# Performance work log

Measured on AMD Instinct MI355X. Metric: run time of the kernel, lower is better.

## Reference

```python
import jax, jax.numpy as jnp
import numpy as np

B, L, ENC_DIM, DEC_DIM, ATTN_DIM = 64, 2048, 1024, 1024, 512


def setup_inputs() -> dict:
    key = jax.random.key(0)
    ks = jax.random.split(key, 8)
    s_enc = 1.0 / np.sqrt(ENC_DIM)
    s_dec = 1.0 / np.sqrt(DEC_DIM)
    s_full = 1.0 / np.sqrt(ATTN_DIM)
    return {
        "encoder_out": jax.random.normal(ks[0], (B, L, ENC_DIM), jnp.float32),
        "decoder_hidden": jax.random.normal(ks[1], (B, DEC_DIM), jnp.float32),
        "We_w": jax.random.uniform(ks[2], (ENC_DIM, ATTN_DIM), jnp.float32, -s_enc, s_enc),
        "We_b": jax.random.uniform(ks[3], (ATTN_DIM,), jnp.float32, -s_enc, s_enc),
        "Wd_w": jax.random.uniform(ks[4], (DEC_DIM, ATTN_DIM), jnp.float32, -s_dec, s_dec),
        "Wd_b": jax.random.uniform(ks[5], (ATTN_DIM,), jnp.float32, -s_dec, s_dec),
        "Wf_w": jax.random.uniform(ks[6], (ATTN_DIM,), jnp.float32, -s_full, s_full),
        "Wf_b": jax.random.uniform(ks[7], (), jnp.float32, -s_full, s_full),
    }


def reference(encoder_out, decoder_hidden, We_w, We_b, Wd_w, Wd_b, Wf_w, Wf_b):
    # enc_attn: [B, L, A]; dec_attn: [B, A]
    enc_attn = jnp.einsum("ble,ea->bla", encoder_out, We_w) + We_b
    dec_attn = decoder_hidden @ Wd_w + Wd_b
    # additive score -> scalar per (B, L)
    hidden = jax.nn.relu(enc_attn + dec_attn[:, None, :])
    attn = jnp.einsum("bla,a->bl", hidden, Wf_w) + Wf_b
    alpha = jax.nn.softmax(attn, axis=1)  # over sequence dim
    weighted = jnp.einsum("ble,bl->be", encoder_out, alpha)
    return (weighted, alpha)
```

## Files before the change

### kernel.cpp

```cpp
#include <hip/hip_runtime.h>
#include <stdint.h>

#define B_BATCH 64
#define L_SEQ 2048
#define E_DIM 1024
#define A_DIM 512

typedef __attribute__((ext_vector_type(4))) float f32x4;
typedef __attribute__((ext_vector_type(8))) short bf16x8;
typedef __attribute__((ext_vector_type(2))) unsigned int u32x2;
typedef __attribute__((ext_vector_type(4))) unsigned int u32x4;

__device__ __forceinline__ unsigned short f2bf(float f) {
  unsigned u = __float_as_uint(f);
  u = (u + 0x7fffu + ((u >> 16) & 1u)) >> 16;
  return (unsigned short)u;
}

__device__ __forceinline__ u32x2 packbf(f32x4 v) {
  u32x2 r;
  r.x = (unsigned)f2bf(v.x) | ((unsigned)f2bf(v.y) << 16);
  r.y = (unsigned)f2bf(v.z) | ((unsigned)f2bf(v.w) << 16);
  return r;
}

#define BUFB 8192
#define BCHUNK 32768

__global__ void prep_we_kernel(const float* __restrict__ We, char* __restrict__ wsB) {
  int t = blockIdx.x * 256 + threadIdx.x;
  int lane = t & 63;
  int colblk = (t >> 6) & 31;
  int step = t >> 11;
  int nl = lane & 15, g = lane >> 4;
  int col = colblk * 16 + nl;
  int k0 = step * 32 + 4 * g;
  unsigned q0 = (unsigned)f2bf(We[(size_t)(k0 + 0) * A_DIM + col]) |
                ((unsigned)f2bf(We[(size_t)(k0 + 1) * A_DIM + col]) << 16);
  unsigned q1 = (unsigned)f2bf(We[(size_t)(k0 + 2) * A_DIM + col]) |
                ((unsigned)f2bf(We[(size_t)(k0 + 3) * A_DIM + col]) << 16);
  unsigned q2 = (unsigned)f2bf(We[(size_t)(k0 + 16) * A_DIM + col]) |
                ((unsigned)f2bf(We[(size_t)(k0 + 17) * A_DIM + col]) << 16);
  unsigned q3 = (unsigned)f2bf(We[(size_t)(k0 + 18) * A_DIM + col]) |
                ((unsigned)f2bf(We[(size_t)(k0 + 19) * A_DIM + col]) << 16);
  u32x4 v; v.x = q0; v.y = q1; v.z = q2; v.w = q3;
  *(u32x4*)(wsB + (size_t)t * 16) = v;
}

__global__ void dec_comb_kernel(const float* __restrict__ dh, const float* __restrict__ Wd,
                                const float* __restrict__ Wdb, const float* __restrict__ Web,
                                float* __restrict__ dcomb) {
  __shared__ float sh[1024];
  const int b = blockIdx.x, tid = threadIdx.x;
  for (int i = tid; i < 1024; i += 256) sh[i] = dh[b * 1024 + i];
  __syncthreads();
  const int a = blockIdx.y * 256 + tid;
  float acc = Wdb[a] + Web[a];
#pragma unroll 4
  for (int e = 0; e < 1024; ++e) acc += sh[e] * Wd[(size_t)e * A_DIM + a];
  dcomb[b * A_DIM + a] = acc;
}

__global__ __launch_bounds__(512, 2) void score_gemm_kernel(
    const float* __restrict__ enc, const char* __restrict__ wsB,
    const float* __restrict__ dcomb, const float* __restrict__ wf,
    float* __restrict__ scoreOut) {
  __shared__ __align__(16) char smem[3 * BUFB];
  __shared__ float s_score[128];

  const int tid = threadIdx.x;
  const int lane = tid & 63;
  const int w = tid >> 6;
  const int g = lane >> 4;
  const int nl = lane & 15;
  const int gs = g ^ ((nl >> 1) & 3);

  const int row0 = (int)blockIdx.x * 128;
  const int bb = row0 >> 11;

  if (tid < 128) s_score[tid] = 0.0f;

  const float* encA = enc + (size_t)row0 * E_DIM;

  int aoff[8];
#pragma unroll
  for (int rt = 0; rt < 8; ++rt) aoff[rt] = (rt * 16 + nl) * 64 + gs * 16;

  const int ar = tid >> 2, ag = tid & 3;
  const int aw = ar * 64 + ((ag ^ ((ar >> 1) & 3)) * 16);
  const float* asrc = encA + (size_t)ar * E_DIM + ag * 4;

  const char* bsrc = wsB + (w * 4) * 1024 + lane * 16;

  f32x4 acc[8][4];
#pragma unroll
  for (int rt = 0; rt < 8; ++rt)
#pragma unroll
    for (int ct = 0; ct < 4; ++ct) {
      f32x4 z = {0.f, 0.f, 0.f, 0.f};
      acc[rt][ct] = z;
    }
  f32x4 ra[2][2];
  bf16x8 bfr[2][4];

#define LOAD_A(kb_, s_)                                  \
  do {                                                   \
    ra[s_][0] = *(const f32x4*)(asrc + (kb_) * 32);      \
    ra[s_][1] = *(const f32x4*)(asrc + (kb_) * 32 + 16); \
  } while (0)

#define LOAD_B(kb_, s_)                                                     \
  do {                                                                      \
    _Pragma("unroll") for (int ct = 0; ct < 4; ++ct) bfr[s_][ct] =          \
        *(const bf16x8*)(bsrc + (size_t)(kb_)*BCHUNK + ct * 1024);          \
  } while (0)

#define WRITE_A(s_, dst_)                                          \
  do {                                                             \
    u32x2 l0 = packbf(ra[s_][0]);                                  \
    u32x2 h0 = packbf(ra[s_][1]);                                  \
    u32x4 w0; w0.x = l0.x; w0.y = l0.y; w0.z = h0.x; w0.w = h0.y;  \
    *(u32x4*)(smem + (dst_) + aw) = w0;                            \
  } while (0)

#define COMPUTE(cur_, s_)                                                    \
  do {                                                                       \
    bf16x8 afr[8];                                                           \
    _Pragma("unroll") for (int rt = 0; rt < 8; ++rt) afr[rt] =               \
        *(const bf16x8*)(smem + (cur_) + aoff[rt]);                          \
    __builtin_amdgcn_s_setprio(1);                                           \
    _Pragma("unroll") for (int rt = 0; rt < 8; ++rt)                         \
        _Pragma("unroll") for (int ct = 0; ct < 4; ++ct) acc[rt][ct] =       \
            __builtin_amdgcn_mfma_f32_16x16x32_bf16(afr[rt], bfr[s_][ct],    \
                                                    acc[rt][ct], 0, 0, 0);   \
    __builtin_amdgcn_s_setprio(0);                                           \
  } while (0)

  LOAD_A(0, 0);
  LOAD_A(1, 1);
  LOAD_B(0, 0);
  asm volatile("s_waitcnt vmcnt(6)" ::: "memory");
  WRITE_A(0, 0);

  int b0 = 0, b1 = BUFB, b2 = 2 * BUFB;
#pragma unroll 6
  for (int t = 0; t < 30; ++t) {
    LOAD_A(t + 2, t & 1);
    LOAD_B(t + 1, (t + 1) & 1);
    asm volatile("s_waitcnt vmcnt(6)" ::: "memory");
    WRITE_A((t + 1) & 1, b1);
    asm volatile("s_waitcnt lgkmcnt(0)" ::: "memory");
    asm volatile("s_barrier" ::: "memory");
    COMPUTE(b0, t & 1);
    int tmp = b0; b0 = b1; b1 = b2; b2 = tmp;
  }
  LOAD_B(31, 1);
  asm volatile("s_waitcnt vmcnt(4)" ::: "memory");
  WRITE_A(1, b1);
  asm volatile("s_waitcnt lgkmcnt(0)" ::: "memory");
  asm volatile("s_barrier" ::: "memory");
  COMPUTE(b0, 0);
  { int tmp = b0; b0 = b1; b1 = b2; b2 = tmp; }
  asm volatile("s_waitcnt vmcnt(0) lgkmcnt(0)" ::: "memory");
  asm volatile("s_barrier" ::: "memory");
  COMPUTE(b0, 1);

#undef LOAD_A
#undef LOAD_B
#undef WRITE_A
#undef COMPUTE

  float db[4], wv[4];
#pragma unroll
  for (int ct = 0; ct < 4; ++ct) {
    int a = w * 64 + ct * 16 + nl;
    db[ct] = dcomb[bb * A_DIM + a];
    wv[ct] = wf[a];
  }
#pragma unroll
  for (int rt = 0; rt < 8; ++rt) {
#pragma unroll
    for (int r = 0; r < 4; ++r) {
      float p = 0.f;
#pragma unroll
      for (int ct = 0; ct < 4; ++ct) {
        float h = acc[rt][ct][r] + db[ct];
        h = h > 0.f ? h : 0.f;
        p += h * wv[ct];
      }
      p += __shfl_xor(p, 1);
      p += __shfl_xor(p, 2);
      p += __shfl_xor(p, 4);
      p += __shfl_xor(p, 8);
      if (nl == 0) atomicAdd(&s_score[rt * 16 + g * 4 + r], p);
    }
  }
  __syncthreads();
  if (tid < 128) scoreOut[row0 + tid] = s_score[tid];
}

__global__ void softmax_kernel(float* __restrict__ attn) {
  __shared__ float red[8];
  const int b = blockIdx.x, tid = threadIdx.x;
  float* p = attn + b * L_SEQ;
  float v[8];
  float m = -1e30f;
#pragma unroll
  for (int i = 0; i < 8; ++i) {
    v[i] = p[tid + i * 256];
    m = fmaxf(m, v[i]);
  }
#pragma unroll
  for (int off = 1; off < 64; off <<= 1) m = fmaxf(m, __shfl_xor(m, off));
  const int wid = tid >> 6;
  if ((tid & 63) == 0) red[wid] = m;
  __syncthreads();
  m = fmaxf(fmaxf(red[0], red[1]), fmaxf(red[2], red[3]));
  float s = 0.f;
#pragma unroll
  for (int i = 0; i < 8; ++i) {
    v[i] = __expf(v[i] - m);
    s += v[i];
  }
#pragma unroll
  for (int off = 1; off < 64; off <<= 1) s += __shfl_xor(s, off);
  __syncthreads();
  if ((tid & 63) == 0) red[4 + wid] = s;
  __syncthreads();
  const float inv = 1.0f / (red[4] + red[5] + red[6] + red[7]);
#pragma unroll
  for (int i = 0; i < 8; ++i) p[tid + i * 256] = v[i] * inv;
}

__global__ void weighted_kernel(const float* __restrict__ enc, const float* __restrict__ alpha,
                                float* __restrict__ outW) {
  __shared__ float sa[64];
  const int bid = blockIdx.x;
  const int b = bid >> 5, ls = bid & 31;
  const int tid = threadIdx.x;
  if (tid < 64) sa[tid] = alpha[b * L_SEQ + ls * 64 + tid];
  __syncthreads();
  const f32x4* ep = (const f32x4*)(enc + ((size_t)(b * L_SEQ + ls * 64)) * E_DIM) + tid;
  f32x4 acc = {0.f, 0.f, 0.f, 0.f};
#pragma unroll 8
  for (int il = 0; il < 64; ++il) {
    f32x4 v = ep[(size_t)il * 256];
    float al = sa[il];
    acc.x += al * v.x;
    acc.y += al * v.y;
    acc.z += al * v.z;
    acc.w += al * v.w;
  }
  float* o = outW + b * E_DIM + tid * 4;
  atomicAdd(o + 0, acc.x);
  atomicAdd(o + 1, acc.y);
  atomicAdd(o + 2, acc.z);
  atomicAdd(o + 3, acc.w);
}

extern "C" void kernel_launch(void* const* d_in, const int* in_sizes, int n_in,
                              void* d_out, int out_size, void* d_ws, size_t ws_size,
                              hipStream_t stream) {
  const float* enc = (const float*)d_in[0];
  const float* dh = (const float*)d_in[1];
  const float* WeW = (const float*)d_in[2];
  const float* WeB = (const float*)d_in[3];
  const float* WdW = (const float*)d_in[4];
  const float* WdB = (const float*)d_in[5];
  const float* WfW = (const float*)d_in[6];

  float* out = (float*)d_out;
  float* outW = out;
  float* attn = out + B_BATCH * E_DIM;

  char* wsB = (char*)d_ws;
  float* dcomb = (float*)((char*)d_ws + 32 * (size_t)BCHUNK);

  if (ws_size < 32 * (size_t)BCHUNK + (size_t)B_BATCH * A_DIM * sizeof(float)) return;

  hipMemsetAsync(outW, 0, (size_t)(B_BATCH * E_DIM) * sizeof(float), stream);
  prep_we_kernel<<<256, 256, 0, stream>>>(WeW, wsB);
  dec_comb_kernel<<<dim3(B_BATCH, 2), 256, 0, stream>>>(dh, WdW, WdB, WeB, dcomb);
  score_gemm_kernel<<<(B_BATCH * L_SEQ) / 128, 512, 0, stream>>>(enc, wsB, dcomb, WfW, attn);
  softmax_kernel<<<B_BATCH, 256, 0, stream>>>(attn);
  weighted_kernel<<<B_BATCH * 32, 256, 0, stream>>>(enc, attn, outW);
}
```

Baseline: 384.5 us.

## Deepen A-tile prefetch to four stages with narrower per-thread enc loads

The score GEMM pipeline moves from three LDS buffers with A prefetched two k-steps ahead to four LDS buffers with A prefetched four k-steps ahead. The per-thread enc load pattern also changes: each thread now loads two 16-byte chunks from rows 64 apart instead of two adjacent chunks, and writes two 8-byte bf16 packs. The aim is to hide more global-load latency on the fp32 encoder stream. In exchange it uses more LDS and registers (ra grows to 4x2 vectors), which could reduce occupancy under launch_bounds(512,2).

```diff
diff --git a/kernel.cpp b/kernel.cpp
--- a/kernel.cpp
+++ b/kernel.cpp
@@ -65,7 +65,7 @@
     const float* __restrict__ enc, const char* __restrict__ wsB,
     const float* __restrict__ dcomb, const float* __restrict__ wf,
     float* __restrict__ scoreOut) {
-  __shared__ __align__(16) char smem[3 * BUFB];
+  __shared__ __align__(16) char smem[4 * BUFB];
   __shared__ float s_score[128];
 
   const int tid = threadIdx.x;
@@ -86,9 +86,10 @@
 #pragma unroll
   for (int rt = 0; rt < 8; ++rt) aoff[rt] = (rt * 16 + nl) * 64 + gs * 16;
 
-  const int ar = tid >> 2, ag = tid & 3;
-  const int aw = ar * 64 + ((ag ^ ((ar >> 1) & 3)) * 16);
-  const float* asrc = encA + (size_t)ar * E_DIM + ag * 4;
+  const int ar = tid >> 3, c = tid & 7;
+  const int aw0 = ar * 64 + (((c & 3) ^ ((ar >> 1) & 3)) * 16) + (c >> 2) * 8;
+  const int aw1 = aw0 + 64 * 64;
+  const float* as0 = encA + (size_t)ar * E_DIM + c * 4;
 
   const char* bsrc = wsB + (w * 4) * 1024 + lane * 16;
 
@@ -100,30 +101,29 @@
       f32x4 z = {0.f, 0.f, 0.f, 0.f};
       acc[rt][ct] = z;
     }
-  f32x4 ra[2][2];
+  f32x4 ra[4][2];
   bf16x8 bfr[2][4];
 
-#define LOAD_A(kb_, s_)                                  \
-  do {                                                   \
-    ra[s_][0] = *(const f32x4*)(asrc + (kb_) * 32);      \
-    ra[s_][1] = *(const f32x4*)(asrc + (kb_) * 32 + 16); \
-  } while (0)
-
-#define LOAD_B(kb_, s_)                                                     \
-  do {                                                                      \
-    _Pragma("unroll") for (int ct = 0; ct < 4; ++ct) bfr[s_][ct] =          \
-        *(const bf16x8*)(bsrc + (size_t)(kb_)*BCHUNK + ct * 1024);          \
-  } while (0)
-
-#define WRITE_A(s_, dst_)                                          \
-  do {                                                             \
-    u32x2 l0 = packbf(ra[s_][0]);                                  \
-    u32x2 h0 = packbf(ra[s_][1]);                                  \
-    u32x4 w0; w0.x = l0.x; w0.y = l0.y; w0.z = h0.x; w0.w = h0.y;  \
-    *(u32x4*)(smem + (dst_) + aw) = w0;                            \
-  } while (0)
-
-#define COMPUTE(cur_, s_)                                                    \
+#define LOAD_A(kb_)                                                     \
+  do {                                                                  \
+    ra[(kb_) & 3][0] = *(const f32x4*)(as0 + (size_t)(kb_) * 32);       \
+    ra[(kb_) & 3][1] = *(const f32x4*)(as0 + (size_t)(kb_) * 32 +       \
+                                       (size_t)64 * E_DIM);             \
+  } while (0)
+
+#define LOAD_B(kb_)                                                     \
+  do {                                                                  \
+    _Pragma("unroll") for (int ct = 0; ct < 4; ++ct) bfr[(kb_) & 1][ct] = \
+        *(const bf16x8*)(bsrc + (size_t)(kb_)*BCHUNK + ct * 1024);      \
+  } while (0)
+
+#define WRITE_A(kb_, dst_)                                              \
+  do {                                                                  \
+    *(u32x2*)(smem + (dst_) + aw0) = packbf(ra[(kb_) & 3][0]);          \
+    *(u32x2*)(smem + (dst_) + aw1) = packbf(ra[(kb_) & 3][1]);          \
+  } while (0)
+
+#define COMPUTE(cur_, kb_)                                                   \
   do {                                                                       \
     bf16x8 afr[8];                                                           \
     _Pragma("unroll") for (int rt = 0; rt < 8; ++rt) afr[rt] =               \
@@ -131,39 +131,50 @@
     __builtin_amdgcn_s_setprio(1);                                           \
     _Pragma("unroll") for (int rt = 0; rt < 8; ++rt)                         \
         _Pragma("unroll") for (int ct = 0; ct < 4; ++ct) acc[rt][ct] =       \
-            __builtin_amdgcn_mfma_f32_16x16x32_bf16(afr[rt], bfr[s_][ct],    \
+            __builtin_amdgcn_mfma_f32_16x16x32_bf16(afr[rt], bfr[(kb_)&1][ct], \
                                                     acc[rt][ct], 0, 0, 0);   \
     __builtin_amdgcn_s_setprio(0);                                           \
   } while (0)
 
-  LOAD_A(0, 0);
-  LOAD_A(1, 1);
-  LOAD_B(0, 0);
-  asm volatile("s_waitcnt vmcnt(6)" ::: "memory");
+  LOAD_A(0);
+  LOAD_B(0);
+  LOAD_A(1);
+  LOAD_A(2);
+  LOAD_A(3);
+  asm volatile("s_waitcnt vmcnt(10)" ::: "memory");
   WRITE_A(0, 0);
 
-  int b0 = 0, b1 = BUFB, b2 = 2 * BUFB;
-#pragma unroll 6
-  for (int t = 0; t < 30; ++t) {
-    LOAD_A(t + 2, t & 1);
-    LOAD_B(t + 1, (t + 1) & 1);
-    asm volatile("s_waitcnt vmcnt(6)" ::: "memory");
-    WRITE_A((t + 1) & 1, b1);
+#pragma unroll 4
+  for (int t = 0; t < 28; ++t) {
+    LOAD_B(t + 1);
+    LOAD_A(t + 4);
+    asm volatile("s_waitcnt vmcnt(8)" ::: "memory");
+    WRITE_A(t + 1, ((t + 1) & 3) * BUFB);
     asm volatile("s_waitcnt lgkmcnt(0)" ::: "memory");
     asm volatile("s_barrier" ::: "memory");
-    COMPUTE(b0, t & 1);
-    int tmp = b0; b0 = b1; b1 = b2; b2 = tmp;
-  }
-  LOAD_B(31, 1);
+    COMPUTE((t & 3) * BUFB, t);
+  }
+  LOAD_B(29);
+  asm volatile("s_waitcnt vmcnt(6)" ::: "memory");
+  WRITE_A(29, 1 * BUFB);
+  asm volatile("s_waitcnt lgkmcnt(0)" ::: "memory");
+  asm volatile("s_barrier" ::: "memory");
+  COMPUTE(0 * BUFB, 28);
+  LOAD_B(30);
   asm volatile("s_waitcnt vmcnt(4)" ::: "memory");
-  WRITE_A(1, b1);
+  WRITE_A(30, 2 * BUFB);
   asm volatile("s_waitcnt lgkmcnt(0)" ::: "memory");
   asm volatile("s_barrier" ::: "memory");
-  COMPUTE(b0, 0);
-  { int tmp = b0; b0 = b1; b1 = b2; b2 = tmp; }
+  COMPUTE(1 * BUFB, 29);
+  LOAD_B(31);
+  asm volatile("s_waitcnt vmcnt(4)" ::: "memory");
+  WRITE_A(31, 3 * BUFB);
+  asm volatile("s_waitcnt lgkmcnt(0)" ::: "memory");
+  asm volatile("s_barrier" ::: "memory");
+  COMPUTE(2 * BUFB, 30);
   asm volatile("s_waitcnt vmcnt(0) lgkmcnt(0)" ::: "memory");
   asm volatile("s_barrier" ::: "memory");
-  COMPUTE(b0, 1);
+  COMPUTE(3 * BUFB, 31);
 
 #undef LOAD_A
 #undef LOAD_B
```

Result: no change. 386.3 us (+0.5%).

## Deepen score GEMM K-step to 64 with split B prefetch and replicated weight copies

Applied to the files above, without the earlier changes.

The score GEMM main loop now stages 64 K-elements of the encoder tile per barrier (two 32-wide chunks per LDS buffer) instead of 32. This halves the number of barriers and interleaves the B-fragment loads between the two MFMA chunks. The prepared bf16 weight buffer is also replicated 8 times in the workspace, and blocks pick a copy by blockIdx, to spread L2/channel contention on the shared weights. The cost is more workspace, a larger LDS footprint (48KB at 2 blocks/CU), and more registers for the A staging.

```diff
diff --git a/kernel.cpp b/kernel.cpp
--- a/kernel.cpp
+++ b/kernel.cpp
@@ -24,8 +24,10 @@
   return r;
 }
 
-#define BUFB 8192
+#define CHUNKB 8192
+#define BUFB 16384
 #define BCHUNK 32768
+#define BCOPY (32 * BCHUNK)
 
 __global__ void prep_we_kernel(const float* __restrict__ We, char* __restrict__ wsB) {
   int t = blockIdx.x * 256 + threadIdx.x;
@@ -44,7 +46,9 @@
   unsigned q3 = (unsigned)f2bf(We[(size_t)(k0 + 18) * A_DIM + col]) |
                 ((unsigned)f2bf(We[(size_t)(k0 + 19) * A_DIM + col]) << 16);
   u32x4 v; v.x = q0; v.y = q1; v.z = q2; v.w = q3;
-  *(u32x4*)(wsB + (size_t)t * 16) = v;
+#pragma unroll
+  for (int c = 0; c < 8; ++c)
+    *(u32x4*)(wsB + (size_t)c * BCOPY + (size_t)t * 16) = v;
 }
 
 __global__ void dec_comb_kernel(const float* __restrict__ dh, const float* __restrict__ Wd,
@@ -86,11 +90,11 @@
 #pragma unroll
   for (int rt = 0; rt < 8; ++rt) aoff[rt] = (rt * 16 + nl) * 64 + gs * 16;
 
-  const int ar = tid >> 2, ag = tid & 3;
-  const int aw = ar * 64 + ((ag ^ ((ar >> 1) & 3)) * 16);
-  const float* asrc = encA + (size_t)ar * E_DIM + ag * 4;
-
-  const char* bsrc = wsB + (w * 4) * 1024 + lane * 16;
+  const int ar = tid >> 2, ac = tid & 3;
+  const int aw = ar * 64 + ((ac ^ ((ar >> 1) & 3)) * 16);
+  const float* asrc = encA + (size_t)ar * E_DIM + ac * 4;
+
+  const char* bsrc = wsB + (size_t)(blockIdx.x & 7) * BCOPY + (w * 4) * 1024 + lane * 16;
 
   f32x4 acc[8][4];
 #pragma unroll
@@ -100,75 +104,87 @@
       f32x4 z = {0.f, 0.f, 0.f, 0.f};
       acc[rt][ct] = z;
     }
-  f32x4 ra[2][2];
-  bf16x8 bfr[2][4];
-
-#define LOAD_A(kb_, s_)                                  \
-  do {                                                   \
-    ra[s_][0] = *(const f32x4*)(asrc + (kb_) * 32);      \
-    ra[s_][1] = *(const f32x4*)(asrc + (kb_) * 32 + 16); \
+  f32x4 ra[4];
+  bf16x8 bfr0[4], bfr1[4];
+
+#define LOAD_A(t_)                                                       \
+  do {                                                                   \
+    _Pragma("unroll") for (int j = 0; j < 4; ++j)                        \
+        ra[j] = *(const f32x4*)(asrc + (size_t)(t_) * 64 + j * 16);      \
   } while (0)
 
-#define LOAD_B(kb_, s_)                                                     \
-  do {                                                                      \
-    _Pragma("unroll") for (int ct = 0; ct < 4; ++ct) bfr[s_][ct] =          \
-        *(const bf16x8*)(bsrc + (size_t)(kb_)*BCHUNK + ct * 1024);          \
+#define LOAD_B(kc_, dst_)                                                \
+  do {                                                                   \
+    _Pragma("unroll") for (int ct = 0; ct < 4; ++ct) dst_[ct] =          \
+        *(const bf16x8*)(bsrc + (size_t)(kc_)*BCHUNK + ct * 1024);       \
   } while (0)
 
-#define WRITE_A(s_, dst_)                                          \
-  do {                                                             \
-    u32x2 l0 = packbf(ra[s_][0]);                                  \
-    u32x2 h0 = packbf(ra[s_][1]);                                  \
-    u32x4 w0; w0.x = l0.x; w0.y = l0.y; w0.z = h0.x; w0.w = h0.y;  \
-    *(u32x4*)(smem + (dst_) + aw) = w0;                            \
+#define WRITE_A(dst_)                                                    \
+  do {                                                                   \
+    u32x2 l0 = packbf(ra[0]), h0 = packbf(ra[1]);                        \
+    u32x2 l1 = packbf(ra[2]), h1 = packbf(ra[3]);                        \
+    u32x4 w0; w0.x = l0.x; w0.y = l0.y; w0.z = h0.x; w0.w = h0.y;        \
+    u32x4 w1; w1.x = l1.x; w1.y = l1.y; w1.z = h1.x; w1.w = h1.y;        \
+    *(u32x4*)(smem + (dst_) + aw) = w0;                                  \
+    *(u32x4*)(smem + (dst_) + CHUNKB + aw) = w1;                         \
   } while (0)
 
-#define COMPUTE(cur_, s_)                                                    \
-  do {                                                                       \
-    bf16x8 afr[8];                                                           \
-    _Pragma("unroll") for (int rt = 0; rt < 8; ++rt) afr[rt] =               \
-        *(const bf16x8*)(smem + (cur_) + aoff[rt]);                          \
-    __builtin_amdgcn_s_setprio(1);                                           \
-    _Pragma("unroll") for (int rt = 0; rt < 8; ++rt)                         \
-        _Pragma("unroll") for (int ct = 0; ct < 4; ++ct) acc[rt][ct] =       \
-            __builtin_amdgcn_mfma_f32_16x16x32_bf16(afr[rt], bfr[s_][ct],    \
-                                                    acc[rt][ct], 0, 0, 0);   \
-    __builtin_amdgcn_s_setprio(0);                                           \
+#define MFMA_CHUNK(cur_, bfr_)                                           \
+  do {                                                                   \
+    bf16x8 afr[8];                                                       \
+    _Pragma("unroll") for (int rt = 0; rt < 8; ++rt) afr[rt] =           \
+        *(const bf16x8*)(smem + (cur_) + aoff[rt]);                      \
+    __builtin_amdgcn_s_setprio(1);                                       \
+    _Pragma("unroll") for (int rt = 0; rt < 8; ++rt)                     \
+        _Pragma("unroll") for (int ct = 0; ct < 4; ++ct) acc[rt][ct] =   \
+            __builtin_amdgcn_mfma_f32_16x16x32_bf16(afr[rt], bfr_[ct],   \
+                                                    acc[rt][ct], 0, 0, 0); \
+    __builtin_amdgcn_s_setprio(0);                                       \
   } while (0)
 
-  LOAD_A(0, 0);
-  LOAD_A(1, 1);
-  LOAD_B(0, 0);
-  asm volatile("s_waitcnt vmcnt(6)" ::: "memory");
-  WRITE_A(0, 0);
+  LOAD_A(0);
+  LOAD_B(0, bfr0);
+  asm volatile("s_waitcnt vmcnt(4)" ::: "memory");
+  WRITE_A(0);
+  LOAD_A(1);
+  asm volatile("s_waitcnt lgkmcnt(0)" ::: "memory");
+  asm volatile("s_barrier" ::: "memory");
 
   int b0 = 0, b1 = BUFB, b2 = 2 * BUFB;
-#pragma unroll 6
-  for (int t = 0; t < 30; ++t) {
-    LOAD_A(t + 2, t & 1);
-    LOAD_B(t + 1, (t + 1) & 1);
-    asm volatile("s_waitcnt vmcnt(6)" ::: "memory");
-    WRITE_A((t + 1) & 1, b1);
+#pragma unroll 2
+  for (int t = 0; t < 14; ++t) {
+    LOAD_B(2 * t + 1, bfr1);
+    asm volatile("s_waitcnt vmcnt(8)" ::: "memory");
+    MFMA_CHUNK(b0, bfr0);
+    LOAD_B(2 * t + 2, bfr0);
+    asm volatile("s_waitcnt vmcnt(4)" ::: "memory");
+    WRITE_A(b1);
+    LOAD_A(t + 2);
     asm volatile("s_waitcnt lgkmcnt(0)" ::: "memory");
     asm volatile("s_barrier" ::: "memory");
-    COMPUTE(b0, t & 1);
+    MFMA_CHUNK(b0 + CHUNKB, bfr1);
     int tmp = b0; b0 = b1; b1 = b2; b2 = tmp;
   }
-  LOAD_B(31, 1);
+  LOAD_B(29, bfr1);
+  asm volatile("s_waitcnt vmcnt(8)" ::: "memory");
+  MFMA_CHUNK(b0, bfr0);
+  LOAD_B(30, bfr0);
   asm volatile("s_waitcnt vmcnt(4)" ::: "memory");
-  WRITE_A(1, b1);
+  WRITE_A(b1);
   asm volatile("s_waitcnt lgkmcnt(0)" ::: "memory");
   asm volatile("s_barrier" ::: "memory");
-  COMPUTE(b0, 0);
+  MFMA_CHUNK(b0 + CHUNKB, bfr1);
   { int tmp = b0; b0 = b1; b1 = b2; b2 = tmp; }
-  asm volatile("s_waitcnt vmcnt(0) lgkmcnt(0)" ::: "memory");
-  asm volatile("s_barrier" ::: "memory");
-  COMPUTE(b0, 1);
+  LOAD_B(31, bfr1);
+  asm volatile("s_waitcnt vmcnt(4)" ::: "memory");
+  MFMA_CHUNK(b0, bfr0);
+  asm volatile("s_waitcnt vmcnt(0)" ::: "memory");
+  MFMA_CHUNK(b0 + CHUNKB, bfr1);
 
 #undef LOAD_A
 #undef LOAD_B
 #undef WRITE_A
-#undef COMPUTE
+#undef MFMA_CHUNK
 
   float db[4], wv[4];
 #pragma unroll
@@ -274,9 +290,9 @@
   float* attn = out + B_BATCH * E_DIM;
 
   char* wsB = (char*)d_ws;
-  float* dcomb = (float*)((char*)d_ws + 32 * (size_t)BCHUNK);
-
-  if (ws_size < 32 * (size_t)BCHUNK + (size_t)B_BATCH * A_DIM * sizeof(float)) return;
+  float* dcomb = (float*)((char*)d_ws + 8 * (size_t)BCOPY);
+
+  if (ws_size < 8 * (size_t)BCOPY + (size_t)B_BATCH * A_DIM * sizeof(float)) return;
 
   hipMemsetAsync(outW, 0, (size_t)(B_BATCH * E_DIM) * sizeof(float), stream);
   prep_we_kernel<<<256, 256, 0, stream>>>(WeW, wsB);
```

Result: no change. 388.1 us (+0.9%).

## Restructure score GEMM A staging into 128-wide K chunks with replicated B copies

Applied to the files above, without the earlier changes.

The score GEMM now stages A in 128-column K blocks split into four 32-wide sub-chunks, double-buffered in LDS. Each sub-chunk's global load, bf16 pack and LDS write is interleaved with MFMAs on the previous block, so there is one barrier per 128 K instead of one per 32. The packed We weights are replicated into 8 workspace copies, chosen by block index, to spread B reads across memory channels and caches. dec_comb is relaunched with 128-thread blocks. The cost is twice as much LDS per block and eight times the workspace for the weight copies.

```diff
diff --git a/kernel.cpp b/kernel.cpp
--- a/kernel.cpp
+++ b/kernel.cpp
@@ -24,8 +24,10 @@
   return r;
 }
 
-#define BUFB 8192
+#define CHUNKB 8192
+#define ABUF (4 * CHUNKB)
 #define BCHUNK 32768
+#define BCOPY (32 * BCHUNK)
 
 __global__ void prep_we_kernel(const float* __restrict__ We, char* __restrict__ wsB) {
   int t = blockIdx.x * 256 + threadIdx.x;
@@ -44,7 +46,9 @@
   unsigned q3 = (unsigned)f2bf(We[(size_t)(k0 + 18) * A_DIM + col]) |
                 ((unsigned)f2bf(We[(size_t)(k0 + 19) * A_DIM + col]) << 16);
   u32x4 v; v.x = q0; v.y = q1; v.z = q2; v.w = q3;
-  *(u32x4*)(wsB + (size_t)t * 16) = v;
+#pragma unroll
+  for (int c = 0; c < 8; ++c)
+    *(u32x4*)(wsB + (size_t)c * BCOPY + (size_t)t * 16) = v;
 }
 
 __global__ void dec_comb_kernel(const float* __restrict__ dh, const float* __restrict__ Wd,
@@ -52,9 +56,9 @@
                                 float* __restrict__ dcomb) {
   __shared__ float sh[1024];
   const int b = blockIdx.x, tid = threadIdx.x;
-  for (int i = tid; i < 1024; i += 256) sh[i] = dh[b * 1024 + i];
-  __syncthreads();
-  const int a = blockIdx.y * 256 + tid;
+  for (int i = tid; i < 1024; i += 128) sh[i] = dh[b * 1024 + i];
+  __syncthreads();
+  const int a = blockIdx.y * 128 + tid;
   float acc = Wdb[a] + Web[a];
 #pragma unroll 4
   for (int e = 0; e < 1024; ++e) acc += sh[e] * Wd[(size_t)e * A_DIM + a];
@@ -65,7 +69,7 @@
     const float* __restrict__ enc, const char* __restrict__ wsB,
     const float* __restrict__ dcomb, const float* __restrict__ wf,
     float* __restrict__ scoreOut) {
-  __shared__ __align__(16) char smem[3 * BUFB];
+  __shared__ __align__(16) char smem[2 * ABUF];
   __shared__ float s_score[128];
 
   const int tid = threadIdx.x;
@@ -81,16 +85,15 @@
   if (tid < 128) s_score[tid] = 0.0f;
 
   const float* encA = enc + (size_t)row0 * E_DIM;
-
-  int aoff[8];
-#pragma unroll
-  for (int rt = 0; rt < 8; ++rt) aoff[rt] = (rt * 16 + nl) * 64 + gs * 16;
-
-  const int ar = tid >> 2, ag = tid & 3;
-  const int aw = ar * 64 + ((ag ^ ((ar >> 1) & 3)) * 16);
-  const float* asrc = encA + (size_t)ar * E_DIM + ag * 4;
-
-  const char* bsrc = wsB + (w * 4) * 1024 + lane * 16;
+  const int anl = nl * 64 + gs * 16;
+
+  const int arow = tid >> 5;
+  const int klq = tid & 31;
+  const float* asrc = encA + (size_t)arow * E_DIM + klq * 4;
+  const int aw_base = (klq >> 3) * CHUNKB + arow * 64 +
+                      (((tid & 3) ^ ((arow >> 1) & 3)) << 4) + ((tid >> 2) & 1) * 8;
+
+  const char* bsrc = wsB + (size_t)(blockIdx.x & 7) * BCOPY + (w * 4) * 1024 + lane * 16;
 
   f32x4 acc[8][4];
 #pragma unroll
@@ -103,72 +106,110 @@
   f32x4 ra[2][2];
   bf16x8 bfr[2][4];
 
-#define LOAD_A(kb_, s_)                                  \
-  do {                                                   \
-    ra[s_][0] = *(const f32x4*)(asrc + (kb_) * 32);      \
-    ra[s_][1] = *(const f32x4*)(asrc + (kb_) * 32 + 16); \
+#define LOAD_P(t_, s_)                                                          \
+  do {                                                                          \
+    ra[(s_) & 1][0] =                                                           \
+        *(const f32x4*)(asrc + (size_t)(2 * (s_)) * 16 * E_DIM + (t_) * 128);   \
+    ra[(s_) & 1][1] =                                                           \
+        *(const f32x4*)(asrc + (size_t)(2 * (s_) + 1) * 16 * E_DIM + (t_) * 128); \
   } while (0)
 
-#define LOAD_B(kb_, s_)                                                     \
-  do {                                                                      \
-    _Pragma("unroll") for (int ct = 0; ct < 4; ++ct) bfr[s_][ct] =          \
-        *(const bf16x8*)(bsrc + (size_t)(kb_)*BCHUNK + ct * 1024);          \
+#define LOAD_B(kcg_, sl_)                                                       \
+  do {                                                                          \
+    _Pragma("unroll") for (int ct = 0; ct < 4; ++ct) bfr[sl_][ct] =             \
+        *(const bf16x8*)(bsrc + (size_t)(kcg_)*BCHUNK + ct * 1024);             \
   } while (0)
 
-#define WRITE_A(s_, dst_)                                          \
-  do {                                                             \
-    u32x2 l0 = packbf(ra[s_][0]);                                  \
-    u32x2 h0 = packbf(ra[s_][1]);                                  \
-    u32x4 w0; w0.x = l0.x; w0.y = l0.y; w0.z = h0.x; w0.w = h0.y;  \
-    *(u32x4*)(smem + (dst_) + aw) = w0;                            \
+#define WRITE_P(s_, nb_)                                                        \
+  do {                                                                          \
+    *(u32x2*)(smem + (nb_) + aw_base + (2 * (s_)) * 1024) = packbf(ra[(s_) & 1][0]); \
+    *(u32x2*)(smem + (nb_) + aw_base + (2 * (s_) + 1) * 1024) =                 \
+        packbf(ra[(s_) & 1][1]);                                                \
   } while (0)
 
-#define COMPUTE(cur_, s_)                                                    \
-  do {                                                                       \
-    bf16x8 afr[8];                                                           \
-    _Pragma("unroll") for (int rt = 0; rt < 8; ++rt) afr[rt] =               \
-        *(const bf16x8*)(smem + (cur_) + aoff[rt]);                          \
-    __builtin_amdgcn_s_setprio(1);                                           \
-    _Pragma("unroll") for (int rt = 0; rt < 8; ++rt)                         \
-        _Pragma("unroll") for (int ct = 0; ct < 4; ++ct) acc[rt][ct] =       \
-            __builtin_amdgcn_mfma_f32_16x16x32_bf16(afr[rt], bfr[s_][ct],    \
-                                                    acc[rt][ct], 0, 0, 0);   \
-    __builtin_amdgcn_s_setprio(0);                                           \
+#define MFMA_CHUNK(cb_, s_, par_)                                               \
+  do {                                                                          \
+    bf16x8 afr[4];                                                              \
+    _Pragma("unroll") for (int rt = 0; rt < 4; ++rt) afr[rt] =                  \
+        *(const bf16x8*)(smem + (cb_) + (s_)*CHUNKB + anl + rt * 1024);         \
+    __builtin_amdgcn_s_setprio(1);                                              \
+    _Pragma("unroll") for (int rt = 0; rt < 4; ++rt)                            \
+        _Pragma("unroll") for (int ct = 0; ct < 4; ++ct) acc[rt][ct] =          \
+            __builtin_amdgcn_mfma_f32_16x16x32_bf16(afr[rt], bfr[par_][ct],     \
+                                                    acc[rt][ct], 0, 0, 0);      \
+    __builtin_amdgcn_s_setprio(0);                                              \
+    _Pragma("unroll") for (int rt = 0; rt < 4; ++rt) afr[rt] =                  \
+        *(const bf16x8*)(smem + (cb_) + (s_)*CHUNKB + anl + (rt + 4) * 1024);   \
+    __builtin_amdgcn_s_setprio(1);                                              \
+    _Pragma("unroll") for (int rt = 0; rt < 4; ++rt)                            \
+        _Pragma("unroll") for (int ct = 0; ct < 4; ++ct) acc[rt + 4][ct] =      \
+            __builtin_amdgcn_mfma_f32_16x16x32_bf16(afr[rt], bfr[par_][ct],     \
+                                                    acc[rt + 4][ct], 0, 0, 0);  \
+    __builtin_amdgcn_s_setprio(0);                                              \
   } while (0)
 
-  LOAD_A(0, 0);
-  LOAD_A(1, 1);
+  LOAD_P(0, 0);
+  LOAD_P(0, 1);
+  asm volatile("s_waitcnt vmcnt(2)" ::: "memory");
+  WRITE_P(0, 0);
+  LOAD_P(0, 2);
+  asm volatile("s_waitcnt vmcnt(2)" ::: "memory");
+  WRITE_P(1, 0);
+  LOAD_P(0, 3);
+  asm volatile("s_waitcnt vmcnt(2)" ::: "memory");
+  WRITE_P(2, 0);
+  asm volatile("s_waitcnt vmcnt(0)" ::: "memory");
+  WRITE_P(3, 0);
   LOAD_B(0, 0);
-  asm volatile("s_waitcnt vmcnt(6)" ::: "memory");
-  WRITE_A(0, 0);
-
-  int b0 = 0, b1 = BUFB, b2 = 2 * BUFB;
-#pragma unroll 6
-  for (int t = 0; t < 30; ++t) {
-    LOAD_A(t + 2, t & 1);
-    LOAD_B(t + 1, (t + 1) & 1);
+  asm volatile("s_waitcnt lgkmcnt(0)" ::: "memory");
+  asm volatile("s_barrier" ::: "memory");
+
+#pragma unroll 1
+  for (int t = 0; t < 7; ++t) {
+    const int cb = (t & 1) * ABUF;
+    const int nb = cb ^ ABUF;
+    LOAD_P(t + 1, 0);
+    LOAD_B(4 * t + 1, 1);
     asm volatile("s_waitcnt vmcnt(6)" ::: "memory");
-    WRITE_A((t + 1) & 1, b1);
+    MFMA_CHUNK(cb, 0, 0);
+    LOAD_P(t + 1, 1);
+    LOAD_B(4 * t + 2, 0);
+    asm volatile("s_waitcnt vmcnt(6)" ::: "memory");
+    WRITE_P(0, nb);
+    MFMA_CHUNK(cb, 1, 1);
+    LOAD_P(t + 1, 2);
+    LOAD_B(4 * t + 3, 1);
+    asm volatile("s_waitcnt vmcnt(6)" ::: "memory");
+    WRITE_P(1, nb);
+    MFMA_CHUNK(cb, 2, 0);
+    LOAD_P(t + 1, 3);
+    LOAD_B(4 * t + 4, 0);
+    asm volatile("s_waitcnt vmcnt(4)" ::: "memory");
+    WRITE_P(2, nb);
+    WRITE_P(3, nb);
+    MFMA_CHUNK(cb, 3, 1);
     asm volatile("s_waitcnt lgkmcnt(0)" ::: "memory");
     asm volatile("s_barrier" ::: "memory");
-    COMPUTE(b0, t & 1);
-    int tmp = b0; b0 = b1; b1 = b2; b2 = tmp;
-  }
-  LOAD_B(31, 1);
-  asm volatile("s_waitcnt vmcnt(4)" ::: "memory");
-  WRITE_A(1, b1);
-  asm volatile("s_waitcnt lgkmcnt(0)" ::: "memory");
-  asm volatile("s_barrier" ::: "memory");
-  COMPUTE(b0, 0);
-  { int tmp = b0; b0 = b1; b1 = b2; b2 = tmp; }
-  asm volatile("s_waitcnt vmcnt(0) lgkmcnt(0)" ::: "memory");
-  asm volatile("s_barrier" ::: "memory");
-  COMPUTE(b0, 1);
-
-#undef LOAD_A
+  }
+  {
+    const int cb = ABUF;
+    LOAD_B(29, 1);
+    asm volatile("s_waitcnt vmcnt(4)" ::: "memory");
+    MFMA_CHUNK(cb, 0, 0);
+    LOAD_B(30, 0);
+    asm volatile("s_waitcnt vmcnt(4)" ::: "memory");
+    MFMA_CHUNK(cb, 1, 1);
+    LOAD_B(31, 1);
+    asm volatile("s_waitcnt vmcnt(4)" ::: "memory");
+    MFMA_CHUNK(cb, 2, 0);
+    asm volatile("s_waitcnt vmcnt(0)" ::: "memory");
+    MFMA_CHUNK(cb, 3, 1);
+  }
+
+#undef LOAD_P
 #undef LOAD_B
-#undef WRITE_A
-#undef COMPUTE
+#undef WRITE_P
+#undef MFMA_CHUNK
 
   float db[4], wv[4];
 #pragma unroll
@@ -240,11 +281,11 @@
   const int tid = threadIdx.x;
   if (tid < 64) sa[tid] = alpha[b * L_SEQ + ls * 64 + tid];
   __syncthreads();
-  const f32x4* ep = (const f32x4*)(enc + ((size_t)(b * L_SEQ + ls * 64)) * E_DIM) + tid;
+  const float* base = enc + ((size_t)(b * L_SEQ + ls * 64)) * E_DIM;
   f32x4 acc = {0.f, 0.f, 0.f, 0.f};
 #pragma unroll 8
   for (int il = 0; il < 64; ++il) {
-    f32x4 v = ep[(size_t)il * 256];
+    f32x4 v = *(const f32x4*)(base + (size_t)il * E_DIM + tid * 4);
     float al = sa[il];
     acc.x += al * v.x;
     acc.y += al * v.y;
@@ -274,13 +315,13 @@
   float* attn = out + B_BATCH * E_DIM;
 
   char* wsB = (char*)d_ws;
-  float* dcomb = (float*)((char*)d_ws + 32 * (size_t)BCHUNK);
-
-  if (ws_size < 32 * (size_t)BCHUNK + (size_t)B_BATCH * A_DIM * sizeof(float)) return;
+  float* dcomb = (float*)((char*)d_ws + 8 * (size_t)BCOPY);
+
+  if (ws_size < 8 * (size_t)BCOPY + (size_t)B_BATCH * A_DIM * sizeof(float)) return;
 
   hipMemsetAsync(outW, 0, (size_t)(B_BATCH * E_DIM) * sizeof(float), stream);
   prep_we_kernel<<<256, 256, 0, stream>>>(WeW, wsB);
-  dec_comb_kernel<<<dim3(B_BATCH, 2), 256, 0, stream>>>(dh, WdW, WdB, WeB, dcomb);
+  dec_comb_kernel<<<dim3(B_BATCH, 4), 128, 0, stream>>>(dh, WdW, WdB, WeB, dcomb);
   score_gemm_kernel<<<(B_BATCH * L_SEQ) / 128, 512, 0, stream>>>(enc, wsB, dcomb, WfW, attn);
   softmax_kernel<<<B_BATCH, 256, 0, stream>>>(attn);
   weighted_kernel<<<B_BATCH * 32, 256, 0, stream>>>(enc, attn, outW);
```

Result: slower. 398.5 us (+3.6%).
